# Kernel optimization log

Measured on AMD Instinct MI355X. Metric: run time of the kernel, lower is better.

Reference implementation:

```python
import jax, jax.numpy as jnp
import numpy as np

B, S, E, H = 4, 2048, 512, 8
D = E // H


def setup_inputs() -> dict:
    key = jax.random.key(0)
    ks = jax.random.split(key, 12)
    sc = 0.02
    return {
        "x": jax.random.normal(ks[0], (B, S, E), jnp.float32),
        "edge_bias": jax.random.normal(ks[1], (B, S, S), jnp.float32),
        "attn_mask": jax.random.randint(ks[2], (B, 1, S, S), 0, 2, jnp.int32),
        "Wq": jax.random.normal(ks[3], (E, E), jnp.float32) * sc,
        "bq": jnp.zeros((E,), jnp.float32),
        "Wk": jax.random.normal(ks[4], (E, E), jnp.float32) * sc,
        "bk": jnp.zeros((E,), jnp.float32),
        "Wv": jax.random.normal(ks[5], (E, E), jnp.float32) * sc,
        "bv": jnp.zeros((E,), jnp.float32),
        "Wo": jax.random.normal(ks[6], (E, E), jnp.float32) * sc,
        "bo": jnp.zeros((E,), jnp.float32),
    }


def reference(x, edge_bias, attn_mask, Wq, bq, Wk, bk, Wv, bv, Wo, bo):
    scale = D ** -0.5
    # projections -> [B, H, S, D]
    def proj(W, b):
        return (x @ W.T + b).reshape(B, S, H, D).transpose(0, 2, 1, 3)
    q = proj(Wq, bq)
    k = proj(Wk, bk)
    v = proj(Wv, bv)
    # scores [B, H, S, S] with edge bias and mask before softmax
    scores = jnp.einsum("bhqd,bhkd->bhqk", q, k) * scale
    scores = scores + edge_bias[:, None, :, :]
    scores = jnp.where(attn_mask == 0, -jnp.inf, scores)
    probs = jax.nn.softmax(scores, axis=-1)
    out = jnp.einsum("bhqk,bhkd->bhqd", probs, v)
    out = out.transpose(0, 2, 1, 3).reshape(B, S, E)
    return out @ Wo.T + bo
```

## Files before the change

kernel.cpp:

```cpp
#include <hip/hip_runtime.h>
#include <hip/hip_bf16.h>
#include <stdint.h>

#define DEV static __device__ __forceinline__

typedef float f32x4 __attribute__((ext_vector_type(4)));
typedef int   i32x4 __attribute__((ext_vector_type(4)));
typedef unsigned short u16x4 __attribute__((ext_vector_type(4)));
typedef unsigned u32x4 __attribute__((ext_vector_type(4)));
typedef __bf16 bf16x8 __attribute__((ext_vector_type(8)));

constexpr int Bb = 4, Ss = 2048, Ee = 512, Hh = 8, Dd = 64;
constexpr float LOG2E = 1.4426950408889634f;

DEV unsigned short f2bf(float f) {
  unsigned u = __float_as_uint(f);
  u += 0x7fff + ((u >> 16) & 1);
  return (unsigned short)(u >> 16);
}

DEV unsigned cvtpk(float lo, float hi) {
  unsigned r;
  asm("v_cvt_pk_bf16_f32 %0, %1, %2" : "=v"(r) : "v"(lo), "v"(hi));
  return r;
}

DEV void gload16(const void* g, void* l) {
  __builtin_amdgcn_global_load_lds((__attribute__((address_space(1))) void*)(g),
                                   (__attribute__((address_space(3))) void*)(l), 16, 0, 0);
}

__global__ void k_cvt(const float* __restrict__ src, unsigned short* __restrict__ dst, int n4) {
  int i = blockIdx.x * 256 + threadIdx.x;
  if (i >= n4) return;
  f32x4 v = *(const f32x4*)(src + (size_t)i * 4);
  u16x4 o;
#pragma unroll
  for (int j = 0; j < 4; ++j) o[j] = f2bf(v[j]);
  *(u16x4*)(dst + (size_t)i * 4) = o;
}

__global__ void k_mb(const float* __restrict__ bias, const int* __restrict__ mask,
                     unsigned short* __restrict__ mb, int n4) {
  int i = blockIdx.x * 256 + threadIdx.x;
  if (i >= n4) return;
  f32x4 v = *(const f32x4*)(bias + (size_t)i * 4);
  i32x4 m = *(const i32x4*)(mask + (size_t)i * 4);
  u16x4 o;
  const unsigned short NEG = f2bf(-1e38f * LOG2E);
#pragma unroll
  for (int j = 0; j < 4; ++j) o[j] = m[j] ? f2bf(v[j] * LOG2E) : NEG;
  *(u16x4*)(mb + (size_t)i * 4) = o;
}

template <int MODE>
__global__ __launch_bounds__(256) void k_gemm(
    const unsigned short* __restrict__ A, const unsigned short* __restrict__ Bw,
    const float* __restrict__ b0, const float* __restrict__ b1, const float* __restrict__ b2,
    unsigned short* __restrict__ oq, unsigned short* __restrict__ ok,
    unsigned short* __restrict__ ovt, float* __restrict__ of32) {
  __shared__ unsigned short Asl[128 * 32];
  __shared__ unsigned short Bsl[128 * 32];
  const int tid = threadIdx.x;
  const int wave = tid >> 6, lane = tid & 63;
  const int l15 = lane & 15, lg = lane >> 4;
  const int brow = blockIdx.x, bcol = blockIdx.y;
  const int wm = (wave >> 1) * 64, wn = (wave & 1) * 64;

  f32x4 acc[4][4] = {};

  for (int k0 = 0; k0 < 512; k0 += 32) {
    __syncthreads();
#pragma unroll
    for (int rnd = 0; rnd < 2; ++rnd) {
      int vid = rnd * 256 + tid;
      int r = vid >> 2, c = vid & 3;
      gload16(A + (size_t)(brow * 128 + r) * 512 + k0 + c * 8,
              Asl + (size_t)(rnd * 256 + wave * 64) * 8);
      gload16(Bw + (size_t)(bcol * 128 + r) * 512 + k0 + c * 8,
              Bsl + (size_t)(rnd * 256 + wave * 64) * 8);
    }
    __syncthreads();
    bf16x8 af[4], bfr[4];
#pragma unroll
    for (int m = 0; m < 4; ++m) af[m] = *(const bf16x8*)(Asl + (wm + m * 16 + l15) * 32 + lg * 8);
#pragma unroll
    for (int n = 0; n < 4; ++n) bfr[n] = *(const bf16x8*)(Bsl + (wn + n * 16 + l15) * 32 + lg * 8);
#pragma unroll
    for (int m = 0; m < 4; ++m)
#pragma unroll
      for (int n = 0; n < 4; ++n)
        acc[m][n] = __builtin_amdgcn_mfma_f32_16x16x32_bf16(af[m], bfr[n], acc[m][n], 0, 0, 0);
  }

  if (MODE == 0) {
    const int Nbase = bcol * 128;
    const int mat = Nbase >> 9;
    const int colb = Nbase & 511;
    const float* bp = (mat == 0) ? b0 : ((mat == 1) ? b1 : b2);
#pragma unroll
    for (int m = 0; m < 4; ++m)
#pragma unroll
      for (int n = 0; n < 4; ++n) {
        const int col = colb + wn + n * 16 + l15;
        const int h = col >> 6, d = col & 63;
        const float bv = bp[col];
#pragma unroll
        for (int j = 0; j < 4; ++j) {
          const int M = brow * 128 + wm + m * 16 + lg * 4 + j;
          const int b = M >> 11, s = M & 2047;
          float outv = acc[m][n][j] + bv;
          if (mat == 0) outv *= 0.125f * LOG2E;
          const unsigned short hv = f2bf(outv);
          if (mat == 0)
            oq[(((size_t)(b * Hh + h)) * Ss + s) * Dd + d] = hv;
          else if (mat == 1)
            ok[(((size_t)(b * Hh + h)) * Ss + s) * Dd + d] = hv;
          else
            ovt[(((size_t)(b * Hh + h)) * Dd + d) * Ss + s] = hv;
        }
      }
  } else {
#pragma unroll
    for (int m = 0; m < 4; ++m)
#pragma unroll
      for (int n = 0; n < 4; ++n) {
        const int col = bcol * 128 + wn + n * 16 + l15;
        const float bv = b0[col];
#pragma unroll
        for (int j = 0; j < 4; ++j) {
          const int M = brow * 128 + wm + m * 16 + lg * 4 + j;
          of32[(size_t)M * 512 + col] = acc[m][n][j] + bv;
        }
      }
  }
}

__global__ __launch_bounds__(256, 4) void k_attn(
    const unsigned short* __restrict__ q, const unsigned short* __restrict__ k,
    const unsigned short* __restrict__ vt, const unsigned short* __restrict__ mb,
    unsigned short* __restrict__ att) {
  __shared__ unsigned short Ksl[2][4096];
  __shared__ unsigned short Vsl[2][4096];
  const int tid = threadIdx.x;
  const int wave = tid >> 6, lane = tid & 63;
  const int l15 = lane & 15, lg = lane >> 4;
  const int bid = blockIdx.x;
  const int xcd = bid & 7, slot = bid >> 3;
  const int bh = (xcd << 2) | (slot >> 5);
  const int qt = slot & 31;
  const int b = bh >> 3, h = bh & 7;
  const size_t qkb = (size_t)bh * Ss * Dd;
  const size_t vtbase = (size_t)bh * Dd * Ss;
  const int q0 = qt * 64 + wave * 16;
  const int qrow = q0 + l15;

  const int addrA = (l15 + 32 * (lg & 1)) * 4;
  const int addrB = addrA + 64;
  const bool hi = (lg >> 1) != 0;
  const int lgs8 = (lg ^ ((l15 >> 1) & 3)) * 8;

  bf16x8 qf[2];
#pragma unroll
  for (int ks = 0; ks < 2; ++ks)
    qf[ks] = *(const bf16x8*)(q + qkb + (size_t)qrow * Dd + ks * 32 + lg * 8);

  const size_t mbrow = ((size_t)b * Ss + qrow) * Ss + lg * 4;

  const unsigned one2 = 0x3F803F80u;
  u32x4 ow; ow[0] = one2; ow[1] = one2; ow[2] = one2; ow[3] = one2;
  const bf16x8 onesv = __builtin_bit_cast(bf16x8, ow);

  f32x4 accO[4] = {};
  f32x4 accL = {};
  float mrow = -INFINITY;

  {
#pragma unroll
    for (int rnd = 0; rnd < 2; ++rnd) {
      int v2 = rnd * 256 + tid;
      int ks = v2 >> 8, r = (v2 >> 2) & 63, c = v2 & 3;
      int cs = c ^ ((r >> 1) & 3);
      gload16(k + qkb + (size_t)r * Dd + ks * 32 + cs * 8,
              &Ksl[0][(rnd * 256 + wave * 64) * 8]);
    }
#pragma unroll
    for (int rnd = 0; rnd < 2; ++rnd) {
      int v2 = rnd * 256 + tid;
      int ks = v2 >> 8, r = (v2 >> 2) & 63, c = v2 & 3;
      int cs = c ^ ((r >> 1) & 3);
      gload16(vt + vtbase + (size_t)r * Ss + ks * 32 + cs * 8,
              &Vsl[0][(rnd * 256 + wave * 64) * 8]);
    }
  }
  u16x4 bvv[4];
#pragma unroll
  for (int m = 0; m < 4; ++m) bvv[m] = *(const u16x4*)(mb + mbrow + m * 16);

  for (int t = 0; t < 32; ++t) {
    const int cur = t & 1;
    __syncthreads();

    f32x4 binit[4];
#pragma unroll
    for (int m = 0; m < 4; ++m)
#pragma unroll
      for (int j = 0; j < 4; ++j)
        binit[m][j] = __uint_as_float(((unsigned)bvv[m][j]) << 16);

    if (t < 31) {
      const int key0 = (t + 1) * 64;
#pragma unroll
      for (int rnd = 0; rnd < 2; ++rnd) {
        int v2 = rnd * 256 + tid;
        int ks = v2 >> 8, r = (v2 >> 2) & 63, c = v2 & 3;
        int cs = c ^ ((r >> 1) & 3);
        gload16(k + qkb + (size_t)(key0 + r) * Dd + ks * 32 + cs * 8,
                &Ksl[cur ^ 1][(rnd * 256 + wave * 64) * 8]);
      }
#pragma unroll
      for (int rnd = 0; rnd < 2; ++rnd) {
        int v2 = rnd * 256 + tid;
        int ks = v2 >> 8, r = (v2 >> 2) & 63, c = v2 & 3;
        int cs = c ^ ((r >> 1) & 3);
        gload16(vt + vtbase + (size_t)r * Ss + key0 + ks * 32 + cs * 8,
                &Vsl[cur ^ 1][(rnd * 256 + wave * 64) * 8]);
      }
#pragma unroll
      for (int m = 0; m < 4; ++m)
        bvv[m] = *(const u16x4*)(mb + mbrow + key0 + m * 16);
    }

    f32x4 sc[4];
    {
      bf16x8 kfm[4];
#pragma unroll
      for (int m = 0; m < 4; ++m)
        kfm[m] = *(const bf16x8*)(&Ksl[cur][(m * 16 + l15) * 32 + lgs8]);
#pragma unroll
      for (int m = 0; m < 4; ++m)
        sc[m] = __builtin_amdgcn_mfma_f32_16x16x32_bf16(kfm[m], qf[0], binit[m], 0, 0, 0);
#pragma unroll
      for (int m = 0; m < 4; ++m)
        kfm[m] = *(const bf16x8*)(&Ksl[cur][2048 + (m * 16 + l15) * 32 + lgs8]);
#pragma unroll
      for (int m = 0; m < 4; ++m)
        sc[m] = __builtin_amdgcn_mfma_f32_16x16x32_bf16(kfm[m], qf[1], sc[m], 0, 0, 0);
    }

    float mm[4];
#pragma unroll
    for (int m = 0; m < 4; ++m)
      mm[m] = fmaxf(fmaxf(fmaxf(sc[m][0], sc[m][1]), sc[m][2]), sc[m][3]);
    float pm = fmaxf(fmaxf(fmaxf(mm[0], mm[1]), mm[2]), mm[3]);
    pm = fmaxf(pm, __shfl_xor(pm, 16));
    pm = fmaxf(pm, __shfl_xor(pm, 32));
    const float mnew = fmaxf(mrow, pm);
    if (!__all(pm <= mrow)) {
      const float c = exp2f(mrow - mnew);
#pragma unroll
      for (int n = 0; n < 4; ++n) accO[n] *= c;
      accL *= c;
    }
    mrow = mnew;

#pragma unroll
    for (int m = 0; m < 4; ++m)
#pragma unroll
      for (int j = 0; j < 4; ++j)
        sc[m][j] = exp2f(sc[m][j] - mnew);

    unsigned pk[4][2];
#pragma unroll
    for (int m = 0; m < 4; ++m) {
      pk[m][0] = cvtpk(sc[m][0], sc[m][1]);
      pk[m][1] = cvtpk(sc[m][2], sc[m][3]);
    }

#pragma unroll
    for (int ks2 = 0; ks2 < 2; ++ks2) {
      bf16x8 va[4];
#pragma unroll
      for (int n = 0; n < 4; ++n)
        va[n] = *(const bf16x8*)(&Vsl[cur][ks2 * 2048 + (n * 16 + l15) * 32 + lgs8]);
      const int mlo = 2 * ks2, mhi = 2 * ks2 + 1;
      unsigned lo0 = __builtin_amdgcn_ds_bpermute(addrA, pk[mlo][0]);
      unsigned hi0 = __builtin_amdgcn_ds_bpermute(addrA, pk[mhi][0]);
      unsigned lo1 = __builtin_amdgcn_ds_bpermute(addrA, pk[mlo][1]);
      unsigned hi1 = __builtin_amdgcn_ds_bpermute(addrA, pk[mhi][1]);
      unsigned lo2 = __builtin_amdgcn_ds_bpermute(addrB, pk[mlo][0]);
      unsigned hi2 = __builtin_amdgcn_ds_bpermute(addrB, pk[mhi][0]);
      unsigned lo3 = __builtin_amdgcn_ds_bpermute(addrB, pk[mlo][1]);
      unsigned hi3 = __builtin_amdgcn_ds_bpermute(addrB, pk[mhi][1]);
      u32x4 wv;
      wv[0] = hi ? hi0 : lo0;
      wv[1] = hi ? hi1 : lo1;
      wv[2] = hi ? hi2 : lo2;
      wv[3] = hi ? hi3 : lo3;
      const bf16x8 pB = __builtin_bit_cast(bf16x8, wv);
#pragma unroll
      for (int n = 0; n < 4; ++n)
        accO[n] = __builtin_amdgcn_mfma_f32_16x16x32_bf16(va[n], pB, accO[n], 0, 0, 0);
      accL = __builtin_amdgcn_mfma_f32_16x16x32_bf16(onesv, pB, accL, 0, 0, 0);
    }
  }

  const float invl = 1.0f / accL[0];
#pragma unroll
  for (int n = 0; n < 4; ++n) {
    u16x4 o;
#pragma unroll
    for (int j = 0; j < 4; ++j) o[j] = f2bf(accO[n][j] * invl);
    *(u16x4*)(att + ((size_t)b * Ss + qrow) * Ee + h * Dd + n * 16 + lg * 4) = o;
  }
}

extern "C" void kernel_launch(void* const* d_in, const int* in_sizes, int n_in,
                              void* d_out, int out_size, void* d_ws, size_t ws_size,
                              hipStream_t stream) {
  const float* x  = (const float*)d_in[0];
  const float* eb = (const float*)d_in[1];
  const int*   am = (const int*)d_in[2];
  const float* Wq = (const float*)d_in[3];
  const float* bq = (const float*)d_in[4];
  const float* Wk = (const float*)d_in[5];
  const float* bk = (const float*)d_in[6];
  const float* Wv = (const float*)d_in[7];
  const float* bv = (const float*)d_in[8];
  const float* Wo = (const float*)d_in[9];
  const float* bo = (const float*)d_in[10];
  float* out = (float*)d_out;

  unsigned short* xb   = (unsigned short*)d_ws;
  unsigned short* wqkv = xb + (size_t)8192 * 512;
  unsigned short* wo   = wqkv + (size_t)1536 * 512;
  unsigned short* qb   = wo + (size_t)512 * 512;
  unsigned short* kb   = qb + (size_t)Bb * Hh * Ss * Dd;
  unsigned short* vtb  = kb + (size_t)Bb * Hh * Ss * Dd;
  unsigned short* attb = vtb + (size_t)Bb * Hh * Ss * Dd;
  unsigned short* mbb  = attb + (size_t)8192 * 512;

  k_cvt<<<4096, 256, 0, stream>>>(x, xb, 8192 * 512 / 4);
  k_cvt<<<256, 256, 0, stream>>>(Wq, wqkv, 512 * 512 / 4);
  k_cvt<<<256, 256, 0, stream>>>(Wk, wqkv + (size_t)512 * 512, 512 * 512 / 4);
  k_cvt<<<256, 256, 0, stream>>>(Wv, wqkv + (size_t)1024 * 512, 512 * 512 / 4);
  k_cvt<<<256, 256, 0, stream>>>(Wo, wo, 512 * 512 / 4);
  k_mb<<<16384, 256, 0, stream>>>(eb, am, mbb, Bb * Ss * Ss / 4);

  dim3 blk(256);
  dim3 g1(64, 12);
  k_gemm<0><<<g1, blk, 0, stream>>>(xb, wqkv, bq, bk, bv, qb, kb, vtb, nullptr);
  k_attn<<<1024, blk, 0, stream>>>(qb, kb, vtb, mbb, attb);
  dim3 g3(64, 4);
  k_gemm<1><<<g3, blk, 0, stream>>>(attb, wo, bo, nullptr, nullptr, nullptr, nullptr, nullptr, out);
}
```

Before: 181.7 us.

## Process two 16-row query groups per wave in attention to reuse K/V fragments

Each wave in the attention kernel now handles 32 query rows (two groups of 16) instead of 16, so each block covers 128 queries and the grid is halved. K and V fragments read from LDS, and each K/V tile loaded from global memory, are reused across both query groups, which cuts LDS and global traffic per unit of MFMA work. MFMA sections are wrapped in s_setprio. The cost is more registers per thread (launch bounds lowered to 2 blocks) and fewer blocks in flight, which may hurt latency hiding and load balance.

Measured after the change: 172.4 us. -5.2%, faster.

```diff
diff --git a/kernel.cpp b/kernel.cpp
--- a/kernel.cpp
+++ b/kernel.cpp
@@ -136,7 +136,7 @@
   }
 }
 
-__global__ __launch_bounds__(256, 4) void k_attn(
+__global__ __launch_bounds__(256, 2) void k_attn(
     const unsigned short* __restrict__ q, const unsigned short* __restrict__ k,
     const unsigned short* __restrict__ vt, const unsigned short* __restrict__ mb,
     unsigned short* __restrict__ att) {
@@ -147,33 +147,37 @@
   const int l15 = lane & 15, lg = lane >> 4;
   const int bid = blockIdx.x;
   const int xcd = bid & 7, slot = bid >> 3;
-  const int bh = (xcd << 2) | (slot >> 5);
-  const int qt = slot & 31;
+  const int bh = (xcd << 2) | (slot >> 4);
+  const int qt = slot & 15;
   const int b = bh >> 3, h = bh & 7;
   const size_t qkb = (size_t)bh * Ss * Dd;
   const size_t vtbase = (size_t)bh * Dd * Ss;
-  const int q0 = qt * 64 + wave * 16;
-  const int qrow = q0 + l15;
+  const int q0 = qt * 128 + wave * 32;
 
   const int addrA = (l15 + 32 * (lg & 1)) * 4;
   const int addrB = addrA + 64;
   const bool hi = (lg >> 1) != 0;
   const int lgs8 = (lg ^ ((l15 >> 1) & 3)) * 8;
 
-  bf16x8 qf[2];
-#pragma unroll
-  for (int ks = 0; ks < 2; ++ks)
-    qf[ks] = *(const bf16x8*)(q + qkb + (size_t)qrow * Dd + ks * 32 + lg * 8);
-
-  const size_t mbrow = ((size_t)b * Ss + qrow) * Ss + lg * 4;
+  bf16x8 qf[2][2];
+#pragma unroll
+  for (int g = 0; g < 2; ++g)
+#pragma unroll
+    for (int ks = 0; ks < 2; ++ks)
+      qf[g][ks] = *(const bf16x8*)(q + qkb + (size_t)(q0 + g * 16 + l15) * Dd + ks * 32 + lg * 8);
+
+  size_t mbrow[2];
+#pragma unroll
+  for (int g = 0; g < 2; ++g)
+    mbrow[g] = ((size_t)b * Ss + (q0 + g * 16 + l15)) * Ss + lg * 4;
 
   const unsigned one2 = 0x3F803F80u;
   u32x4 ow; ow[0] = one2; ow[1] = one2; ow[2] = one2; ow[3] = one2;
   const bf16x8 onesv = __builtin_bit_cast(bf16x8, ow);
 
-  f32x4 accO[4] = {};
-  f32x4 accL = {};
-  float mrow = -INFINITY;
+  f32x4 accO[2][4] = {};
+  f32x4 accL[2] = {};
+  float mrow0 = -INFINITY, mrow1 = -INFINITY;
 
   {
 #pragma unroll
@@ -193,20 +197,25 @@
               &Vsl[0][(rnd * 256 + wave * 64) * 8]);
     }
   }
-  u16x4 bvv[4];
-#pragma unroll
-  for (int m = 0; m < 4; ++m) bvv[m] = *(const u16x4*)(mb + mbrow + m * 16);
+  u16x4 bvv[2][4];
+#pragma unroll
+  for (int g = 0; g < 2; ++g)
+#pragma unroll
+    for (int m = 0; m < 4; ++m)
+      bvv[g][m] = *(const u16x4*)(mb + mbrow[g] + m * 16);
 
   for (int t = 0; t < 32; ++t) {
     const int cur = t & 1;
     __syncthreads();
 
-    f32x4 binit[4];
-#pragma unroll
-    for (int m = 0; m < 4; ++m)
-#pragma unroll
-      for (int j = 0; j < 4; ++j)
-        binit[m][j] = __uint_as_float(((unsigned)bvv[m][j]) << 16);
+    f32x4 binit[2][4];
+#pragma unroll
+    for (int g = 0; g < 2; ++g)
+#pragma unroll
+      for (int m = 0; m < 4; ++m)
+#pragma unroll
+        for (int j = 0; j < 4; ++j)
+          binit[g][m][j] = __uint_as_float(((unsigned)bvv[g][m][j]) << 16);
 
     if (t < 31) {
       const int key0 = (t + 1) * 64;
@@ -227,55 +236,81 @@
                 &Vsl[cur ^ 1][(rnd * 256 + wave * 64) * 8]);
       }
 #pragma unroll
-      for (int m = 0; m < 4; ++m)
-        bvv[m] = *(const u16x4*)(mb + mbrow + key0 + m * 16);
-    }
-
-    f32x4 sc[4];
+      for (int g = 0; g < 2; ++g)
+#pragma unroll
+        for (int m = 0; m < 4; ++m)
+          bvv[g][m] = *(const u16x4*)(mb + mbrow[g] + key0 + m * 16);
+    }
+
+    f32x4 sc[2][4];
     {
       bf16x8 kfm[4];
 #pragma unroll
       for (int m = 0; m < 4; ++m)
         kfm[m] = *(const bf16x8*)(&Ksl[cur][(m * 16 + l15) * 32 + lgs8]);
-#pragma unroll
-      for (int m = 0; m < 4; ++m)
-        sc[m] = __builtin_amdgcn_mfma_f32_16x16x32_bf16(kfm[m], qf[0], binit[m], 0, 0, 0);
+      __builtin_amdgcn_s_setprio(1);
+#pragma unroll
+      for (int g = 0; g < 2; ++g)
+#pragma unroll
+        for (int m = 0; m < 4; ++m)
+          sc[g][m] = __builtin_amdgcn_mfma_f32_16x16x32_bf16(kfm[m], qf[g][0], binit[g][m], 0, 0, 0);
+      __builtin_amdgcn_s_setprio(0);
 #pragma unroll
       for (int m = 0; m < 4; ++m)
         kfm[m] = *(const bf16x8*)(&Ksl[cur][2048 + (m * 16 + l15) * 32 + lgs8]);
-#pragma unroll
-      for (int m = 0; m < 4; ++m)
-        sc[m] = __builtin_amdgcn_mfma_f32_16x16x32_bf16(kfm[m], qf[1], sc[m], 0, 0, 0);
-    }
-
-    float mm[4];
+      __builtin_amdgcn_s_setprio(1);
+#pragma unroll
+      for (int g = 0; g < 2; ++g)
+#pragma unroll
+        for (int m = 0; m < 4; ++m)
+          sc[g][m] = __builtin_amdgcn_mfma_f32_16x16x32_bf16(kfm[m], qf[g][1], sc[g][m], 0, 0, 0);
+      __builtin_amdgcn_s_setprio(0);
+    }
+
+    float pm0, pm1;
+    {
+      float a0 = fmaxf(fmaxf(fmaxf(sc[0][0][0], sc[0][0][1]), sc[0][0][2]), sc[0][0][3]);
+      float a1 = fmaxf(fmaxf(fmaxf(sc[0][1][0], sc[0][1][1]), sc[0][1][2]), sc[0][1][3]);
+      float a2 = fmaxf(fmaxf(fmaxf(sc[0][2][0], sc[0][2][1]), sc[0][2][2]), sc[0][2][3]);
+      float a3 = fmaxf(fmaxf(fmaxf(sc[0][3][0], sc[0][3][1]), sc[0][3][2]), sc[0][3][3]);
+      pm0 = fmaxf(fmaxf(a0, a1), fmaxf(a2, a3));
+      float b0 = fmaxf(fmaxf(fmaxf(sc[1][0][0], sc[1][0][1]), sc[1][0][2]), sc[1][0][3]);
+      float b1 = fmaxf(fmaxf(fmaxf(sc[1][1][0], sc[1][1][1]), sc[1][1][2]), sc[1][1][3]);
+      float b2 = fmaxf(fmaxf(fmaxf(sc[1][2][0], sc[1][2][1]), sc[1][2][2]), sc[1][2][3]);
+      float b3 = fmaxf(fmaxf(fmaxf(sc[1][3][0], sc[1][3][1]), sc[1][3][2]), sc[1][3][3]);
+      pm1 = fmaxf(fmaxf(b0, b1), fmaxf(b2, b3));
+    }
+    pm0 = fmaxf(pm0, __shfl_xor(pm0, 16));
+    pm0 = fmaxf(pm0, __shfl_xor(pm0, 32));
+    pm1 = fmaxf(pm1, __shfl_xor(pm1, 16));
+    pm1 = fmaxf(pm1, __shfl_xor(pm1, 32));
+    const float mnew0 = fmaxf(mrow0, pm0);
+    const float mnew1 = fmaxf(mrow1, pm1);
+    if (!__all(pm0 <= mrow0 && pm1 <= mrow1)) {
+      const float c0 = exp2f(mrow0 - mnew0);
+      const float c1 = exp2f(mrow1 - mnew1);
+#pragma unroll
+      for (int n = 0; n < 4; ++n) { accO[0][n] *= c0; accO[1][n] *= c1; }
+      accL[0] *= c0; accL[1] *= c1;
+    }
+    mrow0 = mnew0; mrow1 = mnew1;
+
 #pragma unroll
     for (int m = 0; m < 4; ++m)
-      mm[m] = fmaxf(fmaxf(fmaxf(sc[m][0], sc[m][1]), sc[m][2]), sc[m][3]);
-    float pm = fmaxf(fmaxf(fmaxf(mm[0], mm[1]), mm[2]), mm[3]);
-    pm = fmaxf(pm, __shfl_xor(pm, 16));
-    pm = fmaxf(pm, __shfl_xor(pm, 32));
-    const float mnew = fmaxf(mrow, pm);
-    if (!__all(pm <= mrow)) {
-      const float c = exp2f(mrow - mnew);
-#pragma unroll
-      for (int n = 0; n < 4; ++n) accO[n] *= c;
-      accL *= c;
-    }
-    mrow = mnew;
-
-#pragma unroll
-    for (int m = 0; m < 4; ++m)
-#pragma unroll
-      for (int j = 0; j < 4; ++j)
-        sc[m][j] = exp2f(sc[m][j] - mnew);
-
-    unsigned pk[4][2];
-#pragma unroll
-    for (int m = 0; m < 4; ++m) {
-      pk[m][0] = cvtpk(sc[m][0], sc[m][1]);
-      pk[m][1] = cvtpk(sc[m][2], sc[m][3]);
-    }
+#pragma unroll
+      for (int j = 0; j < 4; ++j) {
+        sc[0][m][j] = exp2f(sc[0][m][j] - mnew0);
+        sc[1][m][j] = exp2f(sc[1][m][j] - mnew1);
+      }
+
+    unsigned pk[2][4][2];
+#pragma unroll
+    for (int g = 0; g < 2; ++g)
+#pragma unroll
+      for (int m = 0; m < 4; ++m) {
+        pk[g][m][0] = cvtpk(sc[g][m][0], sc[g][m][1]);
+        pk[g][m][1] = cvtpk(sc[g][m][2], sc[g][m][3]);
+      }
 
 #pragma unroll
     for (int ks2 = 0; ks2 < 2; ++ks2) {
@@ -284,34 +319,62 @@
       for (int n = 0; n < 4; ++n)
         va[n] = *(const bf16x8*)(&Vsl[cur][ks2 * 2048 + (n * 16 + l15) * 32 + lgs8]);
       const int mlo = 2 * ks2, mhi = 2 * ks2 + 1;
-      unsigned lo0 = __builtin_amdgcn_ds_bpermute(addrA, pk[mlo][0]);
-      unsigned hi0 = __builtin_amdgcn_ds_bpermute(addrA, pk[mhi][0]);
-      unsigned lo1 = __builtin_amdgcn_ds_bpermute(addrA, pk[mlo][1]);
-      unsigned hi1 = __builtin_amdgcn_ds_bpermute(addrA, pk[mhi][1]);
-      unsigned lo2 = __builtin_amdgcn_ds_bpermute(addrB, pk[mlo][0]);
-      unsigned hi2 = __builtin_amdgcn_ds_bpermute(addrB, pk[mhi][0]);
-      unsigned lo3 = __builtin_amdgcn_ds_bpermute(addrB, pk[mlo][1]);
-      unsigned hi3 = __builtin_amdgcn_ds_bpermute(addrB, pk[mhi][1]);
-      u32x4 wv;
-      wv[0] = hi ? hi0 : lo0;
-      wv[1] = hi ? hi1 : lo1;
-      wv[2] = hi ? hi2 : lo2;
-      wv[3] = hi ? hi3 : lo3;
-      const bf16x8 pB = __builtin_bit_cast(bf16x8, wv);
-#pragma unroll
-      for (int n = 0; n < 4; ++n)
-        accO[n] = __builtin_amdgcn_mfma_f32_16x16x32_bf16(va[n], pB, accO[n], 0, 0, 0);
-      accL = __builtin_amdgcn_mfma_f32_16x16x32_bf16(onesv, pB, accL, 0, 0, 0);
+      bf16x8 pB0, pB1;
+      {
+        unsigned lo0 = __builtin_amdgcn_ds_bpermute(addrA, pk[0][mlo][0]);
+        unsigned hi0 = __builtin_amdgcn_ds_bpermute(addrA, pk[0][mhi][0]);
+        unsigned lo1 = __builtin_amdgcn_ds_bpermute(addrA, pk[0][mlo][1]);
+        unsigned hi1 = __builtin_amdgcn_ds_bpermute(addrA, pk[0][mhi][1]);
+        unsigned lo2 = __builtin_amdgcn_ds_bpermute(addrB, pk[0][mlo][0]);
+        unsigned hi2 = __builtin_amdgcn_ds_bpermute(addrB, pk[0][mhi][0]);
+        unsigned lo3 = __builtin_amdgcn_ds_bpermute(addrB, pk[0][mlo][1]);
+        unsigned hi3 = __builtin_amdgcn_ds_bpermute(addrB, pk[0][mhi][1]);
+        u32x4 wv;
+        wv[0] = hi ? hi0 : lo0;
+        wv[1] = hi ? hi1 : lo1;
+        wv[2] = hi ? hi2 : lo2;
+        wv[3] = hi ? hi3 : lo3;
+        pB0 = __builtin_bit_cast(bf16x8, wv);
+      }
+      {
+        unsigned lo0 = __builtin_amdgcn_ds_bpermute(addrA, pk[1][mlo][0]);
+        unsigned hi0 = __builtin_amdgcn_ds_bpermute(addrA, pk[1][mhi][0]);
+        unsigned lo1 = __builtin_amdgcn_ds_bpermute(addrA, pk[1][mlo][1]);
+        unsigned hi1 = __builtin_amdgcn_ds_bpermute(addrA, pk[1][mhi][1]);
+        unsigned lo2 = __builtin_amdgcn_ds_bpermute(addrB, pk[1][mlo][0]);
+        unsigned hi2 = __builtin_amdgcn_ds_bpermute(addrB, pk[1][mhi][0]);
+        unsigned lo3 = __builtin_amdgcn_ds_bpermute(addrB, pk[1][mlo][1]);
+        unsigned hi3 = __builtin_amdgcn_ds_bpermute(addrB, pk[1][mhi][1]);
+        u32x4 wv;
+        wv[0] = hi ? hi0 : lo0;
+        wv[1] = hi ? hi1 : lo1;
+        wv[2] = hi ? hi2 : lo2;
+        wv[3] = hi ? hi3 : lo3;
+        pB1 = __builtin_bit_cast(bf16x8, wv);
+      }
+      __builtin_amdgcn_s_setprio(1);
+#pragma unroll
+      for (int n = 0; n < 4; ++n) {
+        accO[0][n] = __builtin_amdgcn_mfma_f32_16x16x32_bf16(va[n], pB0, accO[0][n], 0, 0, 0);
+        accO[1][n] = __builtin_amdgcn_mfma_f32_16x16x32_bf16(va[n], pB1, accO[1][n], 0, 0, 0);
+      }
+      accL[0] = __builtin_amdgcn_mfma_f32_16x16x32_bf16(onesv, pB0, accL[0], 0, 0, 0);
+      accL[1] = __builtin_amdgcn_mfma_f32_16x16x32_bf16(onesv, pB1, accL[1], 0, 0, 0);
+      __builtin_amdgcn_s_setprio(0);
     }
   }
 
-  const float invl = 1.0f / accL[0];
-#pragma unroll
-  for (int n = 0; n < 4; ++n) {
-    u16x4 o;
-#pragma unroll
-    for (int j = 0; j < 4; ++j) o[j] = f2bf(accO[n][j] * invl);
-    *(u16x4*)(att + ((size_t)b * Ss + qrow) * Ee + h * Dd + n * 16 + lg * 4) = o;
+#pragma unroll
+  for (int g = 0; g < 2; ++g) {
+    const float invl = 1.0f / accL[g][0];
+    const int qrow = q0 + g * 16 + l15;
+#pragma unroll
+    for (int n = 0; n < 4; ++n) {
+      u16x4 o;
+#pragma unroll
+      for (int j = 0; j < 4; ++j) o[j] = f2bf(accO[g][n][j] * invl);
+      *(u16x4*)(att + ((size_t)b * Ss + qrow) * Ee + h * Dd + n * 16 + lg * 4) = o;
+    }
   }
 }
 
@@ -350,7 +413,7 @@
   dim3 blk(256);
   dim3 g1(64, 12);
   k_gemm<0><<<g1, blk, 0, stream>>>(xb, wqkv, bq, bk, bv, qb, kb, vtb, nullptr);
-  k_attn<<<1024, blk, 0, stream>>>(qb, kb, vtb, mbb, attb);
+  k_attn<<<512, blk, 0, stream>>>(qb, kb, vtb, mbb, attb);
   dim3 g3(64, 4);
   k_gemm<1><<<g3, blk, 0, stream>>>(attb, wo, bo, nullptr, nullptr, nullptr, nullptr, nullptr, out);
 }
```
